# Optimization experiments

Hardware: AMD Instinct MI355X
Metric: run time of the kernel (lower is better)

Reference implementation:

```python
import jax, jax.numpy as jnp
import numpy as np

K = 3
STRIDE = 1
PAD = 1


def setup_inputs() -> dict:
    key = jax.random.key(0)
    k1, k2, k3 = jax.random.split(key, 3)
    N, C, H, W = 4, 256, 64, 64
    outC = 256
    x = jax.random.normal(k1, (N, C, H, W), dtype=jnp.float32)
    # offset/mask conv params (torch inits these to 0; small random makes the test nontrivial)
    conv_offset_w = jax.random.normal(k2, (3 * K * K, C, K, K), dtype=jnp.float32) * 0.01
    conv_offset_b = jnp.zeros((3 * K * K,), dtype=jnp.float32)
    # xavier-normal scale for dcn weight
    fan = C * K * K + outC * K * K
    dcn_weight = jax.random.normal(k3, (outC, C, K, K), dtype=jnp.float32) * np.float32(np.sqrt(2.0 / fan))
    return {"x": x, "conv_offset_w": conv_offset_w, "conv_offset_b": conv_offset_b, "dcn_weight": dcn_weight}


def _dcn(x, w_off, b_off, dcn_weight):
    k, s, p = K, STRIDE, PAD
    N, C, H, W = x.shape
    outC = dcn_weight.shape[0]
    KK = k * k
    # offset/mask prediction conv
    om = jax.lax.conv_general_dilated(
        x, w_off, (s, s), [(p, p), (p, p)],
        dimension_numbers=("NCHW", "OIHW", "NCHW")) + b_off[None, :, None, None]
    offset = om[:, : 2 * KK]
    mask = jax.nn.sigmoid(om[:, 2 * KK:])
    oH = (H + 2 * p - (k - 1)) // s
    oW = (W + 2 * p - (k - 1)) // s
    # pad with an extra row/col at bottom-right so floor+1 indexing is in-bounds (as in torch code)
    px = jnp.pad(x, ((0, 0), (0, 0), (p, p + 1), (p, p + 1)))
    px = jnp.transpose(px, (0, 2, 3, 1))  # (N, H+2p+1, W+2p+1, C)
    offset = jnp.transpose(offset, (0, 2, 3, 1)).reshape(N, oH, oW, KK, 2)  # (...,(y,x))
    mask = jnp.transpose(mask, (0, 2, 3, 1))  # (N, oH, oW, KK)
    base_y = jnp.arange(oH, dtype=jnp.float32) * s + p
    base_x = jnp.arange(oW, dtype=jnp.float32) * s + p
    half = (k - 1) // 2
    inner_y = jnp.repeat(jnp.arange(k, dtype=jnp.float32) - half, k)  # kernel-tap y offsets
    inner_x = jnp.tile(jnp.arange(k, dtype=jnp.float32) - half, k)   # kernel-tap x offsets
    pos_y = base_y[None, :, None, None] + inner_y[None, None, None, :] + offset[..., 0]
    pos_x = base_x[None, None, :, None] + inner_x[None, None, None, :] + offset[..., 1]
    pos_y = jnp.clip(pos_y, 0.0, H + 2 * p - 1.0)
    pos_x = jnp.clip(pos_x, 0.0, W + 2 * p - 1.0)
    y1 = jnp.floor(pos_y)
    x1 = jnp.floor(pos_x)
    y1i = y1.astype(jnp.int32)
    x1i = x1.astype(jnp.int32)
    nidx = jnp.arange(N)[:, None, None, None]
    # bilinear gathers: each (N, oH, oW, KK, C)
    v1 = px[nidx, y1i, x1i]
    v2 = px[nidx, y1i, x1i + 1]
    v3 = px[nidx, y1i + 1, x1i]
    v4 = px[nidx, y1i + 1, x1i + 1]
    lh = (pos_y - y1)[..., None]
    lw = (pos_x - x1)[..., None]
    hh = 1.0 - lh
    hw = 1.0 - lw
    value = hh * hw * v1 + hh * lw * v2 + lh * hw * v3 + lh * lw * v4
    value = value * mask[..., None]  # modulated
    w = dcn_weight.reshape(outC, C, KK)
    # sum over in_C and kernel taps -> NCHW output
    out = jnp.einsum("nhwkc,ock->nohw", value, w)
    return out


def reference(x, conv_offset_w, conv_offset_b, dcn_weight):
    return _dcn(x, conv_offset_w, conv_offset_b, dcn_weight)
```

## Files before the change

kernel.cpp:

```cpp
#include <hip/hip_runtime.h>
#include <type_traits>


typedef __bf16 bf16x8 __attribute__((ext_vector_type(8)));
typedef float  f32x4  __attribute__((ext_vector_type(4)));
typedef unsigned short ushort8 __attribute__((ext_vector_type(8)));
typedef unsigned short ushort4v __attribute__((ext_vector_type(4)));
typedef unsigned int   uint2v  __attribute__((ext_vector_type(2)));

#define XBF_OFF   0u
#define WREP_OFF  8388608u
#define WMAIN_OFF 8536064u
#define OM_OFF    9715712u

#define LGKM0_BAR() do { __builtin_amdgcn_s_waitcnt(0xC07F); __builtin_amdgcn_s_barrier(); } while (0)

template <int N> using ic = std::integral_constant<int, N>;

__device__ __forceinline__ unsigned short f2bf(float f) {
  unsigned int u = __float_as_uint(f);
  u += 0x7fffu + ((u >> 16) & 1u);
  return (unsigned short)(u >> 16);
}
__device__ __forceinline__ float bf2f(unsigned short h) {
  return __uint_as_float(((unsigned int)h) << 16);
}

__global__ __launch_bounds__(256) void k_pre(const float* __restrict__ x,
                                             const float* __restrict__ w_off,
                                             const float* __restrict__ dcn_w,
                                             unsigned short* __restrict__ xbf,
                                             unsigned short* __restrict__ wrep,
                                             unsigned short* __restrict__ wmain) {
  __shared__ float tile[32][65];
  __shared__ unsigned short lsh[2304];
  int b = blockIdx.x;
  int t = threadIdx.x;
  if (b < 2048) {
    int n  = b >> 9;
    int cb = (b >> 6) & 7;
    int xb = b & 63;
    int xx  = t & 63;
    int cc0 = t >> 6;
#pragma unroll
    for (int j = 0; j < 8; ++j) {
      int cc = cc0 + j * 4;
      tile[cc][xx] = x[((size_t)(n * 256 + cb * 32 + cc) << 12) + xb * 64 + xx];
    }
    __syncthreads();
    int ccw = t & 31;
    int xw0 = t >> 5;
#pragma unroll
    for (int j = 0; j < 8; ++j) {
      int xw = xw0 + j * 8;
      xbf[((size_t)((n << 12) + xb * 64 + xw)) * 256 + cb * 32 + ccw] = f2bf(tile[ccw][xw]);
    }
  } else {
    int ocb = b - 2048;
    if (ocb < 32) {
      int oc = ocb;
      if (oc >= 27) {
#pragma unroll
        for (int j = 0; j < 9; ++j) wrep[oc * 2304 + j * 256 + t] = 0;
        return;
      }
      const float* base = w_off + (size_t)oc * 2304;
#pragma unroll
      for (int j = 0; j < 9; ++j) lsh[j * 256 + t] = f2bf(base[t * 9 + j]);
      __syncthreads();
#pragma unroll
      for (int j = 0; j < 9; ++j) wrep[oc * 2304 + j * 256 + t] = lsh[j * 256 + t];
    } else {
      int oc = ocb - 32;
      const float* base = dcn_w + (size_t)oc * 2304;
      int oco = ((oc >> 4) << 9) + (oc & 15) * 8;
#pragma unroll
      for (int j = 0; j < 9; ++j) {
        int k = j * 256 + t;
        wmain[((k >> 5) << 13) + oco + (((k >> 3) & 3) << 7) + (k & 7)] =
            f2bf(base[t * 9 + j]);
      }
    }
  }
}

__global__ __launch_bounds__(1024) void k_offconv(const unsigned short* __restrict__ xbf,
                                                  const unsigned short* __restrict__ wrep,
                                                  const float* __restrict__ bias,
                                                  float* __restrict__ om) {
  __shared__ __align__(16) unsigned short SHa[4][64 * 64];
  __shared__ __align__(16) unsigned short SHb[4][32 * 64];
  int t = threadIdx.x;
  int wave = t >> 6, lane = t & 63;
  int grp = wave >> 2, wv = wave & 3;
  int tg = t & 255;
  int bm = ((blockIdx.x & 7) << 5) + (blockIdx.x >> 3);
  int n = bm >> 6, oy = bm & 63;

  unsigned short* As = SHa[grp];
  unsigned short* Bs = SHb[grp];

  int arow = tg >> 2, acc4 = tg & 3;
  int brow = tg >> 3, bch = tg & 7;

  f32x4 acc0 = {0.f, 0.f, 0.f, 0.f};
  f32x4 acc1 = {0.f, 0.f, 0.f, 0.f};

  ushort8 av[2][2]; ushort8 bv[2];
  auto prefetch = [&](int ktg, auto slotc) {
    constexpr int slot = decltype(slotc)::value;
    int kk = ktg >> 2;
    int c0 = (ktg & 3) * 64;
    int dy = kk / 3 - 1, dx = kk % 3 - 1;
    int yy = oy + dy, xxg = arow + dx;
    bool ok = ((unsigned)yy < 64u) && ((unsigned)xxg < 64u);
    const unsigned short* p = xbf + (size_t)(((n * 64 + yy) * 64 + xxg) * 256 + c0 + acc4 * 16);
#pragma unroll
    for (int g = 0; g < 2; ++g)
      av[slot][g] = ok ? *(const ushort8*)(p + g * 8) : (ushort8){0,0,0,0,0,0,0,0};
    bv[slot] = *(const ushort8*)(wrep + (size_t)brow * 2304 + ktg * 64 + bch * 8);
  };

  int k0 = grp * 9;
  prefetch(k0, ic<0>{});
  prefetch(k0 + 1, ic<1>{});
  int mr = lane & 15, q = lane >> 4;

  auto step = [&](int kt, auto slotc) {
    constexpr int slot = decltype(slotc)::value;
    LGKM0_BAR();
#pragma unroll
    for (int g = 0; g < 2; ++g) {
      int ch = (acc4 * 2 + g) ^ (arow & 7);
      *(ushort8*)&As[arow * 64 + ch * 8] = av[slot][g];
    }
    { int ch = bch ^ (brow & 7);
      *(ushort8*)&Bs[brow * 64 + ch * 8] = bv[slot]; }
    if (kt + 2 < 9) prefetch(k0 + kt + 2, slotc);
    LGKM0_BAR();
#pragma unroll
    for (int kh = 0; kh < 2; ++kh) {
      int coff = ((q + kh * 4) ^ (mr & 7)) * 8;
      bf16x8 a  = *(const bf16x8*)&As[(wv * 16 + mr) * 64 + coff];
      bf16x8 b0 = *(const bf16x8*)&Bs[mr * 64 + coff];
      bf16x8 b1 = *(const bf16x8*)&Bs[(16 + mr) * 64 + coff];
      acc0 = __builtin_amdgcn_mfma_f32_16x16x32_bf16(a, b0, acc0, 0, 0, 0);
      acc1 = __builtin_amdgcn_mfma_f32_16x16x32_bf16(a, b1, acc1, 0, 0, 0);
    }
  };
  for (int kp = 0; kp < 4; ++kp) {
    step(2 * kp, ic<0>{});
    step(2 * kp + 1, ic<1>{});
  }
  step(8, ic<0>{});

  float* scratch = (float*)&SHa[0][0];
  __syncthreads();
  if (grp > 0) {
#pragma unroll
    for (int nt = 0; nt < 2; ++nt) {
      f32x4 a = nt ? acc1 : acc0;
#pragma unroll
      for (int rg = 0; rg < 4; ++rg)
        scratch[(grp - 1) * 2048 + (wv * 16 + q * 4 + rg) * 32 + nt * 16 + mr] = a[rg];
    }
  }
  __syncthreads();
  if (grp == 0) {
    int r0 = bm * 64;
#pragma unroll
    for (int nt = 0; nt < 2; ++nt) {
      f32x4 a = nt ? acc1 : acc0;
      int oc = nt * 16 + mr;
      float bvl = (oc < 27) ? bias[oc] : 0.f;
#pragma unroll
      for (int rg = 0; rg < 4; ++rg) {
        int pl = wv * 16 + q * 4 + rg;
        float v = a[rg] + bvl + scratch[pl * 32 + oc] +
                  scratch[2048 + pl * 32 + oc] + scratch[4096 + pl * 32 + oc];
        if (oc >= 18 && oc < 27) v = 1.f / (1.f + __expf(-v));
        om[(r0 + pl) * 32 + oc] = v;
      }
    }
  }
}

__global__ __launch_bounds__(1024) void k_gemm_fused(const unsigned short* __restrict__ xbf,
                                                     const float* __restrict__ om,
                                                     const unsigned short* __restrict__ wB,
                                                     float* __restrict__ out) {
  __shared__ __align__(16) unsigned short Ab[3][64 * 64];
  int t = threadIdx.x;
  int wave = t >> 6, lane = t & 63;
  int wm = wave & 1, wn = wave >> 1;
  int bmx = ((blockIdx.x & 7) << 5) + (blockIdx.x >> 3);
  int r0 = bmx * 64;

  int srow = t >> 4;
  int sch  = (t & 15) * 4;
  int r = r0 + srow;
  int n = r >> 12, yx = r & 4095, oy = yx >> 6, ox = yx & 63;
  const unsigned short* xb = xbf + (size_t)n * (4096 * 256);
  const float* omr = om + (size_t)r * 32;
  int wch = ((((t >> 1) & 7) ^ (srow & 7)) << 3) + (t & 1) * 4;

  int mr = lane & 15, q = lane >> 4;
  const unsigned short* Bb0 = wB + wn * 1024 + lane * 8;

  f32x4 acc[2][2];
#pragma unroll
  for (int mt = 0; mt < 2; ++mt)
#pragma unroll
    for (int nt = 0; nt < 2; ++nt) acc[mt][nt] = (f32x4){0.f, 0.f, 0.f, 0.f};

  float pv_y, pv_x, pv_m;
  float cw1, cw2, cw3, cw4;
  int a1, a2, a3, a4;
  float wbuf[2][4];

  auto loadom = [&](int kk) {
    pv_y = omr[2 * kk]; pv_x = omr[2 * kk + 1]; pv_m = omr[18 + kk];
  };
  auto params = [&](int kk) {
    float py = (float)(oy + kk / 3) + pv_y;
    float px = (float)(ox + kk % 3) + pv_x;
    float m = pv_m;
    py = fminf(fmaxf(py, 0.f), 65.f);
    px = fminf(fmaxf(px, 0.f), 65.f);
    float fy = floorf(py), fx = floorf(px);
    float ly = py - fy, lx = px - fx;
    float hy = 1.f - ly, hx = 1.f - lx;
    int iy = (int)fy, ix = (int)fx;
    bool yv0 = (iy >= 1) && (iy <= 64);
    bool yv1 = (iy <= 63);
    bool xv0 = (ix >= 1) && (ix <= 64);
    bool xv1 = (ix <= 63);
    int y0 = min(max(iy - 1, 0), 63);
    int y1 = min(iy, 63);
    int x0 = min(max(ix - 1, 0), 63);
    int x1 = min(ix, 63);
    cw1 = (yv0 && xv0) ? hy * hx * m : 0.f;
    cw2 = (yv0 && xv1) ? hy * lx * m : 0.f;
    cw3 = (yv1 && xv0) ? ly * hx * m : 0.f;
    cw4 = (yv1 && xv1) ? ly * lx * m : 0.f;
    a1 = ((y0 << 6) + x0) * 256;
    a2 = ((y0 << 6) + x1) * 256;
    a3 = ((y1 << 6) + x0) * 256;
    a4 = ((y1 << 6) + x1) * 256;
  };

  ushort4v g1[2], g2[2], g3[2], g4[2];
  bf16x8 bfr[2][4];

  auto issueA = [&](int ktg, auto slotc) {
    constexpr int slot = decltype(slotc)::value;
    wbuf[slot][0] = cw1; wbuf[slot][1] = cw2; wbuf[slot][2] = cw3; wbuf[slot][3] = cw4;
    int c = (ktg & 3) * 64 + sch;
    g1[slot] = *(const ushort4v*)(xb + a1 + c);
    g2[slot] = *(const ushort4v*)(xb + a2 + c);
    g3[slot] = *(const ushort4v*)(xb + a3 + c);
    g4[slot] = *(const ushort4v*)(xb + a4 + c);
  };
  auto issueB = [&](int ktg, auto slotc) {
    constexpr int slot = decltype(slotc)::value;
#pragma unroll
    for (int kh = 0; kh < 2; ++kh)
#pragma unroll
      for (int nt = 0; nt < 2; ++nt)
        bfr[slot][kh * 2 + nt] =
            *(const bf16x8*)(Bb0 + (size_t)(ktg * 2 + kh) * 8192 + nt * 512);
  };

  loadom(0);
  params(0);
  loadom(1);
  issueA(0, ic<0>{});
  issueA(1, ic<1>{});
  issueB(0, ic<0>{});

  auto step = [&](int k, auto slotc, auto bufc) {
    constexpr int slot = decltype(slotc)::value;
    constexpr int buf  = decltype(bufc)::value;
    uint2v rs;
#pragma unroll
    for (int p = 0; p < 2; ++p) {
      float va = wbuf[slot][0] * bf2f(g1[slot][2 * p])     + wbuf[slot][1] * bf2f(g2[slot][2 * p]) +
                 wbuf[slot][2] * bf2f(g3[slot][2 * p])     + wbuf[slot][3] * bf2f(g4[slot][2 * p]);
      float vb = wbuf[slot][0] * bf2f(g1[slot][2 * p + 1]) + wbuf[slot][1] * bf2f(g2[slot][2 * p + 1]) +
                 wbuf[slot][2] * bf2f(g3[slot][2 * p + 1]) + wbuf[slot][3] * bf2f(g4[slot][2 * p + 1]);
      unsigned ua = __float_as_uint(va) + 0x8000u;
      unsigned ub = __float_as_uint(vb) + 0x8000u;
      rs[p] = __builtin_amdgcn_perm(ub, ua, 0x07060302u);
    }
    *(uint2v*)&Ab[buf][srow * 64 + wch] = rs;
    if (k + 2 < 36) {
      if (((k + 2) & 3) == 0) {
        int kk = (k + 2) >> 2;
        params(kk);
        loadom(kk < 8 ? kk + 1 : 8);
      }
      issueA(k + 2, slotc);
    }
    if (k + 1 < 36) issueB(k + 1, ic<1 - slot>{});
    LGKM0_BAR();
#pragma unroll
    for (int kh = 0; kh < 2; ++kh) {
      int coff = ((q + kh * 4) ^ (mr & 7)) * 8;
      bf16x8 af0 = *(const bf16x8*)&Ab[buf][(wm * 32 + mr) * 64 + coff];
      bf16x8 af1 = *(const bf16x8*)&Ab[buf][(wm * 32 + 16 + mr) * 64 + coff];
      acc[0][0] = __builtin_amdgcn_mfma_f32_16x16x32_bf16(af0, bfr[slot][kh * 2 + 0], acc[0][0], 0, 0, 0);
      acc[0][1] = __builtin_amdgcn_mfma_f32_16x16x32_bf16(af0, bfr[slot][kh * 2 + 1], acc[0][1], 0, 0, 0);
      acc[1][0] = __builtin_amdgcn_mfma_f32_16x16x32_bf16(af1, bfr[slot][kh * 2 + 0], acc[1][0], 0, 0, 0);
      acc[1][1] = __builtin_amdgcn_mfma_f32_16x16x32_bf16(af1, bfr[slot][kh * 2 + 1], acc[1][1], 0, 0, 0);
    }
  };

  for (int kp = 0; kp < 6; ++kp) {
    int k = kp * 6;
    step(k + 0, ic<0>{}, ic<0>{});
    step(k + 1, ic<1>{}, ic<1>{});
    step(k + 2, ic<0>{}, ic<2>{});
    step(k + 3, ic<1>{}, ic<0>{});
    step(k + 4, ic<0>{}, ic<1>{});
    step(k + 5, ic<1>{}, ic<2>{});
  }

#pragma unroll
  for (int mt = 0; mt < 2; ++mt)
#pragma unroll
    for (int nt = 0; nt < 2; ++nt) {
      int p = r0 + wm * 32 + mt * 16 + q * 4;
      int o = wn * 32 + nt * 16 + mr;
      int nn = p >> 12, pyx = p & 4095;
      *(f32x4*)(out + ((size_t)(nn * 256 + o) << 12) + pyx) = acc[mt][nt];
    }
}

extern "C" void kernel_launch(void* const* d_in, const int* in_sizes, int n_in,
                              void* d_out, int out_size, void* d_ws, size_t ws_size,
                              hipStream_t stream) {
  const float* x     = (const float*)d_in[0];
  const float* w_off = (const float*)d_in[1];
  const float* b_off = (const float*)d_in[2];
  const float* dcn_w = (const float*)d_in[3];
  float* out = (float*)d_out;
  char* ws = (char*)d_ws;
  unsigned short* xbf   = (unsigned short*)(ws + XBF_OFF);
  unsigned short* wrep  = (unsigned short*)(ws + WREP_OFF);
  unsigned short* wmain = (unsigned short*)(ws + WMAIN_OFF);
  float*          om    = (float*)(ws + OM_OFF);

  k_pre<<<2048 + 288, 256, 0, stream>>>(x, w_off, dcn_w, xbf, wrep, wmain);
  k_offconv<<<256, 1024, 0, stream>>>(xbf, wrep, b_off, om);
  k_gemm_fused<<<256, 1024, 0, stream>>>(xbf, om, wmain, out);
}
```

Before: 132.3 us.

## Halve fused GEMM M-tile to 32 rows with 512-thread blocks and 3-deep B prefetch

The fused deformable-gather GEMM now uses 32-row tiles with 8 waves (each covering 32 output channels), launching 512 blocks of 512 threads instead of 256 blocks of 1024. The B-fragment register prefetch becomes three-deep and is indexed by the LDS buffer slot, issued two steps ahead. The aim is better occupancy and more latency hiding across CUs. The cost is that each weight fragment is now reused by half as many rows, so global B traffic per output doubles, and register pressure rises.

```diff
diff --git a/kernel.cpp b/kernel.cpp
--- a/kernel.cpp
+++ b/kernel.cpp
@@ -185,16 +185,16 @@
   }
 }
 
-__global__ __launch_bounds__(1024) void k_gemm_fused(const unsigned short* __restrict__ xbf,
-                                                     const float* __restrict__ om,
-                                                     const unsigned short* __restrict__ wB,
-                                                     float* __restrict__ out) {
-  __shared__ __align__(16) unsigned short Ab[3][64 * 64];
+__global__ __launch_bounds__(512, 4) void k_gemm_fused(const unsigned short* __restrict__ xbf,
+                                                       const float* __restrict__ om,
+                                                       const unsigned short* __restrict__ wB,
+                                                       float* __restrict__ out) {
+  __shared__ __align__(16) unsigned short Ab[3][32 * 64];
   int t = threadIdx.x;
   int wave = t >> 6, lane = t & 63;
-  int wm = wave & 1, wn = wave >> 1;
-  int bmx = ((blockIdx.x & 7) << 5) + (blockIdx.x >> 3);
-  int r0 = bmx * 64;
+  int wn = wave;
+  int bmx = ((blockIdx.x & 7) << 6) + (blockIdx.x >> 3);
+  int r0 = bmx * 32;
 
   int srow = t >> 4;
   int sch  = (t & 15) * 4;
@@ -250,7 +250,7 @@
   };
 
   ushort4v g1[2], g2[2], g3[2], g4[2];
-  bf16x8 bfr[2][4];
+  bf16x8 bfr[3][4];
 
   auto issueA = [&](int ktg, auto slotc) {
     constexpr int slot = decltype(slotc)::value;
@@ -277,17 +277,18 @@
   issueA(0, ic<0>{});
   issueA(1, ic<1>{});
   issueB(0, ic<0>{});
-
-  auto step = [&](int k, auto slotc, auto bufc) {
-    constexpr int slot = decltype(slotc)::value;
-    constexpr int buf  = decltype(bufc)::value;
+  issueB(1, ic<1>{});
+
+  auto step = [&](int k, auto aslotc, auto bufc) {
+    constexpr int aslot = decltype(aslotc)::value;
+    constexpr int buf   = decltype(bufc)::value;
     uint2v rs;
 #pragma unroll
     for (int p = 0; p < 2; ++p) {
-      float va = wbuf[slot][0] * bf2f(g1[slot][2 * p])     + wbuf[slot][1] * bf2f(g2[slot][2 * p]) +
-                 wbuf[slot][2] * bf2f(g3[slot][2 * p])     + wbuf[slot][3] * bf2f(g4[slot][2 * p]);
-      float vb = wbuf[slot][0] * bf2f(g1[slot][2 * p + 1]) + wbuf[slot][1] * bf2f(g2[slot][2 * p + 1]) +
-                 wbuf[slot][2] * bf2f(g3[slot][2 * p + 1]) + wbuf[slot][3] * bf2f(g4[slot][2 * p + 1]);
+      float va = wbuf[aslot][0] * bf2f(g1[aslot][2 * p])     + wbuf[aslot][1] * bf2f(g2[aslot][2 * p]) +
+                 wbuf[aslot][2] * bf2f(g3[aslot][2 * p])     + wbuf[aslot][3] * bf2f(g4[aslot][2 * p]);
+      float vb = wbuf[aslot][0] * bf2f(g1[aslot][2 * p + 1]) + wbuf[aslot][1] * bf2f(g2[aslot][2 * p + 1]) +
+                 wbuf[aslot][2] * bf2f(g3[aslot][2 * p + 1]) + wbuf[aslot][3] * bf2f(g4[aslot][2 * p + 1]);
       unsigned ua = __float_as_uint(va) + 0x8000u;
       unsigned ub = __float_as_uint(vb) + 0x8000u;
       rs[p] = __builtin_amdgcn_perm(ub, ua, 0x07060302u);
@@ -299,19 +300,19 @@
         params(kk);
         loadom(kk < 8 ? kk + 1 : 8);
       }
-      issueA(k + 2, slotc);
-    }
-    if (k + 1 < 36) issueB(k + 1, ic<1 - slot>{});
+      issueA(k + 2, aslotc);
+      issueB(k + 2, ic<(buf + 2) % 3>{});
+    }
     LGKM0_BAR();
 #pragma unroll
     for (int kh = 0; kh < 2; ++kh) {
       int coff = ((q + kh * 4) ^ (mr & 7)) * 8;
-      bf16x8 af0 = *(const bf16x8*)&Ab[buf][(wm * 32 + mr) * 64 + coff];
-      bf16x8 af1 = *(const bf16x8*)&Ab[buf][(wm * 32 + 16 + mr) * 64 + coff];
-      acc[0][0] = __builtin_amdgcn_mfma_f32_16x16x32_bf16(af0, bfr[slot][kh * 2 + 0], acc[0][0], 0, 0, 0);
-      acc[0][1] = __builtin_amdgcn_mfma_f32_16x16x32_bf16(af0, bfr[slot][kh * 2 + 1], acc[0][1], 0, 0, 0);
-      acc[1][0] = __builtin_amdgcn_mfma_f32_16x16x32_bf16(af1, bfr[slot][kh * 2 + 0], acc[1][0], 0, 0, 0);
-      acc[1][1] = __builtin_amdgcn_mfma_f32_16x16x32_bf16(af1, bfr[slot][kh * 2 + 1], acc[1][1], 0, 0, 0);
+      bf16x8 af0 = *(const bf16x8*)&Ab[buf][mr * 64 + coff];
+      bf16x8 af1 = *(const bf16x8*)&Ab[buf][(16 + mr) * 64 + coff];
+      acc[0][0] = __builtin_amdgcn_mfma_f32_16x16x32_bf16(af0, bfr[buf][kh * 2 + 0], acc[0][0], 0, 0, 0);
+      acc[0][1] = __builtin_amdgcn_mfma_f32_16x16x32_bf16(af0, bfr[buf][kh * 2 + 1], acc[0][1], 0, 0, 0);
+      acc[1][0] = __builtin_amdgcn_mfma_f32_16x16x32_bf16(af1, bfr[buf][kh * 2 + 0], acc[1][0], 0, 0, 0);
+      acc[1][1] = __builtin_amdgcn_mfma_f32_16x16x32_bf16(af1, bfr[buf][kh * 2 + 1], acc[1][1], 0, 0, 0);
     }
   };
 
@@ -329,7 +330,7 @@
   for (int mt = 0; mt < 2; ++mt)
 #pragma unroll
     for (int nt = 0; nt < 2; ++nt) {
-      int p = r0 + wm * 32 + mt * 16 + q * 4;
+      int p = r0 + mt * 16 + q * 4;
       int o = wn * 32 + nt * 16 + mr;
       int nn = p >> 12, pyx = p & 4095;
       *(f32x4*)(out + ((size_t)(nn * 256 + o) << 12) + pyx) = acc[mt][nt];
@@ -352,5 +353,5 @@
 
   k_pre<<<2048 + 288, 256, 0, stream>>>(x, w_off, dcn_w, xbf, wrep, wmain);
   k_offconv<<<256, 1024, 0, stream>>>(xbf, wrep, b_off, om);
-  k_gemm_fused<<<256, 1024, 0, stream>>>(xbf, om, wmain, out);
-}
+  k_gemm_fused<<<512, 512, 0, stream>>>(xbf, om, wmain, out);
+}
```

Result: no change. 130.9 us (-1.0%).
